# Performance work log

Measured on AMD Instinct MI355X. Metric: run time of the kernel, lower is better.

Reference implementation:

```python
import jax, jax.numpy as jnp
import numpy as np

N = 50000
E = 800000
D_IN = 64
D_H = 64


def setup_inputs() -> dict:
    key = jax.random.key(0)
    k1, k2, k3, k4 = jax.random.split(key, 4)
    x = jax.random.normal(k1, (N, D_IN), dtype=jnp.float32)
    edge_index = jax.random.randint(k2, (2, E), 0, N, dtype=jnp.int32)
    W1 = jax.random.normal(k3, (D_IN, D_H), dtype=jnp.float32) * (1.0 / np.sqrt(D_IN))
    b1 = jnp.zeros((D_H,), dtype=jnp.float32)
    W2 = jax.random.normal(k4, (D_H, 1), dtype=jnp.float32) * (1.0 / np.sqrt(D_H))
    b2 = jnpp = jnp.zeros((1,), dtype=jnp.float32)
    return {"x": x, "edge_index": edge_index, "W1": W1, "b1": b1, "W2": W2, "b2": b2}


def reference(x, edge_index, W1, b1, W2, b2):
    n = x.shape[0]
    # dgl.add_self_loop: append (i, i) edges for every node
    loops = jnp.arange(n, dtype=edge_index.dtype)
    src = jnp.concatenate([edge_index[0], loops])
    dst = jnp.concatenate([edge_index[1], loops])

    ones = jnp.ones(src.shape[0], dtype=x.dtype)
    deg_out = jax.ops.segment_sum(ones, src, num_segments=n)  # out-degree (src side)
    deg_in = jax.ops.segment_sum(ones, dst, num_segments=n)   # in-degree (dst side)
    # norm='both': symmetric D^{-1/2} A D^{-1/2}; zero where degree is zero (DGL sets inf->0)
    norm_src = jnp.where(deg_out > 0, jax.lax.rsqrt(deg_out), 0.0)[:, None]
    norm_dst = jnp.where(deg_in > 0, jax.lax.rsqrt(deg_in), 0.0)[:, None]

    def aggregate(h):
        # degree-normalized sparse neighbor sum (SpMM via gather + segment_sum)
        h = h * norm_src
        m = jax.ops.segment_sum(h[src], dst, num_segments=n)
        return m * norm_dst

    # layer 1 (in_feats == h_feats -> aggregate first, then transform), bias after agg
    h = aggregate(x) @ W1 + b1
    h = jax.nn.relu(h)
    # layer 2 (in_feats > out_feats -> transform first, then aggregate), bias at end
    out = aggregate(h @ W2) + b2
    return out  # [N, 1]
```

## Files before the change

kernel.cpp:

```cpp
#include <hip/hip_runtime.h>


constexpr int D = 64;
constexpr int NODE_TILE = 12800;
constexpr int NCHUNK = 64;
constexpr int HTH = 1024;

typedef float f32x8 __attribute__((ext_vector_type(8)));

__device__ __forceinline__ int rl_i(int v, int l) { return __builtin_amdgcn_readlane(v, l); }
__device__ __forceinline__ float rl_f(float v, int l) {
    return __builtin_bit_cast(float, __builtin_amdgcn_readlane(__builtin_bit_cast(int, v), l));
}

__global__ void __launch_bounds__(HTH) k_hist_lds(
        const int* __restrict__ src, const int* __restrict__ dst,
        unsigned int* __restrict__ part, int e, int ce) {
    __shared__ unsigned int h[NODE_TILE];
    int b = blockIdx.x;
    int v0 = blockIdx.y * NODE_TILE;
    for (int i = threadIdx.x; i < NODE_TILE; i += HTH) h[i] = 0u;
    __syncthreads();
    int lo = b * ce, hi = min(lo + ce, e);
    for (int i = lo + threadIdx.x; i < hi; i += HTH) {
        unsigned int us = (unsigned int)(src[i] - v0);
        if (us < (unsigned int)NODE_TILE) atomicAdd(&h[us], 1u);
        unsigned int ud = (unsigned int)(dst[i] - v0);
        if (ud < (unsigned int)NODE_TILE) atomicAdd(&h[ud], 0x10000u);
    }
    __syncthreads();
    unsigned int* p = part + ((size_t)blockIdx.y * NCHUNK + b) * NODE_TILE;
    for (int i = threadIdx.x; i < NODE_TILE; i += HTH) p[i] = h[i];
}

__global__ void k_merge(const unsigned int* __restrict__ part,
                        unsigned short* __restrict__ colpref,
                        int* __restrict__ cnt_out, int* __restrict__ cnt_in, int n) {
    int v = blockIdx.x * blockDim.x + threadIdx.x;
    if (v >= n) return;
    int pass = v / NODE_TILE;
    int vl = v - pass * NODE_TILE;
    const unsigned int* p = part + (size_t)pass * NCHUNK * NODE_TILE + vl;
    unsigned int tot = 0, run_in = 0;
    for (int b = 0; b < NCHUNK; ++b) {
        colpref[(size_t)b * n + v] = (unsigned short)run_in;
        unsigned int t = p[(size_t)b * NODE_TILE];
        tot += t;
        run_in += t >> 16;
    }
    cnt_out[v] = (int)(tot & 0xFFFFu);
    cnt_in[v] = (int)(tot >> 16);
}

__global__ void k_scan_block(const int* __restrict__ cnt_in, int* __restrict__ cursor,
                             int* __restrict__ bsum, int n) {
    __shared__ int s[256];
    int tid = threadIdx.x;
    int i = blockIdx.x * 256 + tid;
    int v = (i < n) ? cnt_in[i] : 0;
    s[tid] = v;
    __syncthreads();
#pragma unroll
    for (int off = 1; off < 256; off <<= 1) {
        int t = (tid >= off) ? s[tid - off] : 0;
        __syncthreads();
        s[tid] += t;
        __syncthreads();
    }
    if (i < n) cursor[i] = s[tid] - v;
    if (tid == 255) bsum[blockIdx.x] = s[255];
}

__global__ void k_scan_bsum(int* __restrict__ bsum, int nb) {
    __shared__ int s[256];
    __shared__ int carry;
    int tid = threadIdx.x;
    if (tid == 0) carry = 0;
    __syncthreads();
    for (int start = 0; start < nb; start += 256) {
        int i = start + tid;
        int v = (i < nb) ? bsum[i] : 0;
        s[tid] = v;
        __syncthreads();
#pragma unroll
        for (int off = 1; off < 256; off <<= 1) {
            int t = (tid >= off) ? s[tid - off] : 0;
            __syncthreads();
            s[tid] += t;
            __syncthreads();
        }
        if (i < nb) bsum[i] = s[tid] - v + carry;
        __syncthreads();
        if (tid == 0) carry += s[255];
        __syncthreads();
    }
}

__global__ void k_finalize(const int* __restrict__ cnt_out, const int* __restrict__ cnt_in,
                           const int* __restrict__ bsum,
                           int* __restrict__ cursor, int4* __restrict__ meta, int n) {
    int i = blockIdx.x * blockDim.x + threadIdx.x;
    if (i >= n) return;
    int start = cursor[i] + bsum[i >> 8];
    cursor[i] = start;
    meta[i] = make_int4(start, cnt_in[i], cnt_out[i], 0);
}

__global__ void __launch_bounds__(HTH) k_bin_lds(
        const int* __restrict__ src, const int* __restrict__ dst,
        const int* __restrict__ start, const unsigned short* __restrict__ colpref,
        const int* __restrict__ cnt_out,
        int2* __restrict__ col2, int e, int n, int ce) {
    __shared__ int cur[NODE_TILE];
    int b = blockIdx.x;
    int v0 = blockIdx.y * NODE_TILE;
    int vcnt = min(NODE_TILE, n - v0);
    for (int i = threadIdx.x; i < vcnt; i += HTH)
        cur[i] = start[v0 + i] + (int)colpref[(size_t)b * n + v0 + i];
    __syncthreads();
    int lo = b * ce, hi = min(lo + ce, e);
    for (int i = lo + threadIdx.x; i < hi; i += HTH) {
        int d = dst[i];
        unsigned int ud = (unsigned int)(d - v0);
        if (ud < (unsigned int)NODE_TILE) {
            int s = src[i];
            int p = atomicAdd(&cur[ud], 1);
            float w = rsqrtf((float)(cnt_out[s] + 1));
            col2[p] = make_int2(s, __builtin_bit_cast(int, w));
        }
    }
}

__global__ void __launch_bounds__(256) k_gemm(
        const float* __restrict__ x, const float* __restrict__ W1,
        float* __restrict__ y, int n) {
    __shared__ float sW1[D * D];
    int tid = threadIdx.x;
    for (int i = tid; i < D * D; i += 256) sW1[i] = W1[i];
    __syncthreads();

    int lane = tid & 63;
    int wv = __builtin_amdgcn_readfirstlane(tid >> 6);
    int r0 = (blockIdx.x * 4 + wv) * 8;
    if (r0 >= n) return;

    float acc[8];
#pragma unroll
    for (int i = 0; i < 8; ++i) acc[i] = 0.0f;

    if (r0 + 8 <= n) {
        const float* xw = x + (size_t)r0 * D;
#pragma unroll
        for (int kt = 0; kt < 8; ++kt) {
            const float* p = xw + kt * 8;
            f32x8 X0, X1, X2, X3, X4, X5, X6, X7;
            asm volatile(
                "s_load_dwordx8 %0, %8, 0x0\n\t"
                "s_load_dwordx8 %1, %8, 0x100\n\t"
                "s_load_dwordx8 %2, %8, 0x200\n\t"
                "s_load_dwordx8 %3, %8, 0x300\n\t"
                "s_load_dwordx8 %4, %8, 0x400\n\t"
                "s_load_dwordx8 %5, %8, 0x500\n\t"
                "s_load_dwordx8 %6, %8, 0x600\n\t"
                "s_load_dwordx8 %7, %8, 0x700\n\t"
                "s_waitcnt lgkmcnt(0)"
                : "=s"(X0), "=s"(X1), "=s"(X2), "=s"(X3),
                  "=s"(X4), "=s"(X5), "=s"(X6), "=s"(X7)
                : "s"(p));
#pragma unroll
            for (int j = 0; j < 8; ++j) {
                float wk = sW1[(kt * 8 + j) * D + lane];
                acc[0] = fmaf(X0[j], wk, acc[0]);
                acc[1] = fmaf(X1[j], wk, acc[1]);
                acc[2] = fmaf(X2[j], wk, acc[2]);
                acc[3] = fmaf(X3[j], wk, acc[3]);
                acc[4] = fmaf(X4[j], wk, acc[4]);
                acc[5] = fmaf(X5[j], wk, acc[5]);
                acc[6] = fmaf(X6[j], wk, acc[6]);
                acc[7] = fmaf(X7[j], wk, acc[7]);
            }
        }
#pragma unroll
        for (int i = 0; i < 8; ++i)
            y[(size_t)(r0 + i) * D + lane] = acc[i];
    } else {
        float xr[8];
#pragma unroll
        for (int i = 0; i < 8; ++i) {
            int r = r0 + i;
            xr[i] = (r < n) ? x[(size_t)r * D + lane] : 0.0f;
        }
#pragma unroll
        for (int k = 0; k < D; ++k) {
            float wk = sW1[k * D + lane];
#pragma unroll
            for (int i = 0; i < 8; ++i)
                acc[i] = fmaf(rl_f(xr[i], k), wk, acc[i]);
        }
#pragma unroll
        for (int i = 0; i < 8; ++i) {
            int r = r0 + i;
            if (r < n) y[(size_t)r * D + lane] = acc[i];
        }
    }
}

__global__ void __launch_bounds__(256) k_node(
        const float* __restrict__ y, const int4* __restrict__ meta,
        const int2* __restrict__ col2,
        const float* __restrict__ b1, const float* __restrict__ W2,
        float* __restrict__ zs, int n) {
    int tid = threadIdx.x;
    int wave = tid >> 6;
    int lane = tid & 63;
    float b1v = b1[lane];
    float w2v = W2[lane];

    int nwaves = gridDim.x * 4;
    int node = blockIdx.x * 4 + wave;
    if (node >= n) return;
    int4 mt = meta[node];

    while (true) {
        int nxt = node + nwaves;
        int4 mt_nx = make_int4(0, 0, 0, 0);
        if (nxt < n) mt_nx = meta[nxt];

        int base = mt.x;
        int cnt = mt.y;
        float nd = rsqrtf((float)(mt.y + 1));
        float ns = rsqrtf((float)(mt.z + 1));

        float a0 = ns * y[(size_t)node * D + lane];
        float a1 = 0.0f, a2 = 0.0f, a3 = 0.0f;

        for (int b0 = 0; b0 < cnt; b0 += 64) {
            int m = cnt - b0; if (m > 64) m = 64;
            int2 cw = (lane < m) ? col2[base + b0 + lane] : make_int2(0, 0);
            int idx = cw.x;
            float w = __builtin_bit_cast(float, cw.y);
            int j = 0;
            for (; j + 8 <= m; j += 8) {
                int s0 = rl_i(idx, j + 0), s1 = rl_i(idx, j + 1);
                int s2 = rl_i(idx, j + 2), s3 = rl_i(idx, j + 3);
                int s4 = rl_i(idx, j + 4), s5 = rl_i(idx, j + 5);
                int s6 = rl_i(idx, j + 6), s7 = rl_i(idx, j + 7);
                float x0 = y[(size_t)s0 * D + lane];
                float x1 = y[(size_t)s1 * D + lane];
                float x2 = y[(size_t)s2 * D + lane];
                float x3 = y[(size_t)s3 * D + lane];
                float x4 = y[(size_t)s4 * D + lane];
                float x5 = y[(size_t)s5 * D + lane];
                float x6 = y[(size_t)s6 * D + lane];
                float x7 = y[(size_t)s7 * D + lane];
                a0 = fmaf(rl_f(w, j + 0), x0, a0);
                a1 = fmaf(rl_f(w, j + 1), x1, a1);
                a2 = fmaf(rl_f(w, j + 2), x2, a2);
                a3 = fmaf(rl_f(w, j + 3), x3, a3);
                a0 = fmaf(rl_f(w, j + 4), x4, a0);
                a1 = fmaf(rl_f(w, j + 5), x5, a1);
                a2 = fmaf(rl_f(w, j + 6), x6, a2);
                a3 = fmaf(rl_f(w, j + 7), x7, a3);
            }
            for (; j < m; ++j)
                a0 = fmaf(rl_f(w, j), y[(size_t)rl_i(idx, j) * D + lane], a0);
        }

        float h = fmaxf(((a0 + a1) + (a2 + a3)) * nd + b1v, 0.0f);
        float zp = h * w2v;
#pragma unroll
        for (int off = 32; off > 0; off >>= 1) zp += __shfl_down(zp, off);
        if (lane == 0) zs[node] = zp * ns;

        if (nxt >= n) break;
        node = nxt;
        mt = mt_nx;
    }
}

__global__ void k_out(const float* __restrict__ zs,
                      const int4* __restrict__ meta, const int2* __restrict__ col2,
                      const float* __restrict__ b2,
                      float* __restrict__ out, int n) {
    int g = blockIdx.x * blockDim.x + threadIdx.x;
    int node = g >> 3;
    int sub = g & 7;
    if (node >= n) return;
    int4 mt = meta[node];
    int base = mt.x;
    int c = mt.y;
    float s = (sub == 0) ? zs[node] : 0.0f;
    for (int j = sub; j < c; j += 8) s += zs[col2[base + j].x];
    s += __shfl_xor(s, 1);
    s += __shfl_xor(s, 2);
    s += __shfl_xor(s, 4);
    if (sub == 0) {
        float nd = rsqrtf((float)(mt.y + 1));
        out[node] = nd * s + b2[0];
    }
}

extern "C" void kernel_launch(void* const* d_in, const int* in_sizes, int n_in,
                              void* d_out, int out_size, void* d_ws, size_t ws_size,
                              hipStream_t stream) {
    const float* x  = (const float*)d_in[0];
    const int*   ei = (const int*)d_in[1];
    const float* W1 = (const float*)d_in[2];
    const float* b1 = (const float*)d_in[3];
    const float* W2 = (const float*)d_in[4];
    const float* b2 = (const float*)d_in[5];
    float* out = (float*)d_out;

    const int n = in_sizes[0] / D;
    const int e = in_sizes[1] / 2;
    const int* src = ei;
    const int* dst = ei + e;

    const int nb = (n + 255) / 256;
    const int npass = (n + NODE_TILE - 1) / NODE_TILE;
    const int ce = (e + NCHUNK - 1) / NCHUNK;

    char* ws = (char*)d_ws;
    int*   cnt_out = (int*)ws;   ws += sizeof(int) * (size_t)n;
    int*   cnt_in  = (int*)ws;   ws += sizeof(int) * (size_t)n;
    int*   cursor  = (int*)ws;   ws += sizeof(int) * (size_t)n;
    int*   bsum    = (int*)ws;   ws += sizeof(int) * (size_t)((nb + 255) & ~255);
    int4*  meta    = (int4*)ws;  ws += sizeof(int4) * (size_t)n;
    unsigned short* colpref = (unsigned short*)ws;
    ws += sizeof(unsigned short) * (size_t)NCHUNK * n;
    int2*  col2    = (int2*)ws;  ws += sizeof(int2) * (size_t)e;
    size_t part_bytes = sizeof(unsigned int) * (size_t)npass * NCHUNK * NODE_TILE;
    size_t y_bytes    = sizeof(float) * (size_t)n * D;
    unsigned int* part = (unsigned int*)ws;
    float* y = (float*)ws;
    ws += (part_bytes > y_bytes ? part_bytes : y_bytes);
    float* zs = (float*)cnt_in;

    const int B = 256;

    k_hist_lds<<<dim3(NCHUNK, npass), HTH, 0, stream>>>(src, dst, part, e, ce);
    k_merge<<<(n + B - 1) / B, B, 0, stream>>>(part, colpref, cnt_out, cnt_in, n);
    k_scan_block<<<nb, 256, 0, stream>>>(cnt_in, cursor, bsum, n);
    k_scan_bsum<<<1, 256, 0, stream>>>(bsum, nb);
    k_finalize<<<(n + B - 1) / B, B, 0, stream>>>(cnt_out, cnt_in, bsum, cursor, meta, n);
    k_bin_lds<<<dim3(NCHUNK, npass), HTH, 0, stream>>>(src, dst, cursor, colpref,
                                                       cnt_out, col2, e, n, ce);
    k_gemm<<<(n + 31) / 32, B, 0, stream>>>(x, W1, y, n);
    k_node<<<2048, B, 0, stream>>>(y, meta, col2, b1, W2, zs, n);
    k_out<<<((size_t)n * 8 + B - 1) / B, B, 0, stream>>>(zs, meta, col2, b2, out, n);
}
```

Before: 113.9 us.

## Pack edge source and out-degree into one word; fuse merge with block scan

Replaces the 8-byte (source index, float weight) CSR entries with a 4-byte word: the source node id sits in the low 16 bits and its out-degree in the high 16 bits. The normalization weight is then recomputed with rsqrt inside the aggregation kernel, which halves the edge-list traffic in the bin, node and output kernels. The histogram merge and the per-block prefix scan are also fused into one kernel, removing a launch and a reread of the in-degree counts. The packing assumes node ids and out-degrees fit in 16 bits, which holds for N=50000 but is not general.

```diff
diff --git a/kernel.cpp b/kernel.cpp
--- a/kernel.cpp
+++ b/kernel.cpp
@@ -33,32 +33,30 @@
     for (int i = threadIdx.x; i < NODE_TILE; i += HTH) p[i] = h[i];
 }
 
-__global__ void k_merge(const unsigned int* __restrict__ part,
-                        unsigned short* __restrict__ colpref,
-                        int* __restrict__ cnt_out, int* __restrict__ cnt_in, int n) {
-    int v = blockIdx.x * blockDim.x + threadIdx.x;
-    if (v >= n) return;
-    int pass = v / NODE_TILE;
-    int vl = v - pass * NODE_TILE;
-    const unsigned int* p = part + (size_t)pass * NCHUNK * NODE_TILE + vl;
-    unsigned int tot = 0, run_in = 0;
-    for (int b = 0; b < NCHUNK; ++b) {
-        colpref[(size_t)b * n + v] = (unsigned short)run_in;
-        unsigned int t = p[(size_t)b * NODE_TILE];
-        tot += t;
-        run_in += t >> 16;
-    }
-    cnt_out[v] = (int)(tot & 0xFFFFu);
-    cnt_in[v] = (int)(tot >> 16);
-}
-
-__global__ void k_scan_block(const int* __restrict__ cnt_in, int* __restrict__ cursor,
-                             int* __restrict__ bsum, int n) {
+__global__ void k_merge_scan(const unsigned int* __restrict__ part,
+                             unsigned short* __restrict__ colpref,
+                             int* __restrict__ cnt_out, int* __restrict__ cnt_in,
+                             int* __restrict__ cursor, int* __restrict__ bsum, int n) {
     __shared__ int s[256];
     int tid = threadIdx.x;
-    int i = blockIdx.x * 256 + tid;
-    int v = (i < n) ? cnt_in[i] : 0;
-    s[tid] = v;
+    int v = blockIdx.x * 256 + tid;
+    int ci = 0;
+    if (v < n) {
+        int pass = v / NODE_TILE;
+        int vl = v - pass * NODE_TILE;
+        const unsigned int* p = part + (size_t)pass * NCHUNK * NODE_TILE + vl;
+        unsigned int tot = 0, run_in = 0;
+        for (int b = 0; b < NCHUNK; ++b) {
+            colpref[(size_t)b * n + v] = (unsigned short)run_in;
+            unsigned int t = p[(size_t)b * NODE_TILE];
+            tot += t;
+            run_in += t >> 16;
+        }
+        cnt_out[v] = (int)(tot & 0xFFFFu);
+        ci = (int)(tot >> 16);
+        cnt_in[v] = ci;
+    }
+    s[tid] = ci;
     __syncthreads();
 #pragma unroll
     for (int off = 1; off < 256; off <<= 1) {
@@ -67,7 +65,7 @@
         s[tid] += t;
         __syncthreads();
     }
-    if (i < n) cursor[i] = s[tid] - v;
+    if (v < n) cursor[v] = s[tid] - ci;
     if (tid == 255) bsum[blockIdx.x] = s[255];
 }
 
@@ -110,7 +108,7 @@
         const int* __restrict__ src, const int* __restrict__ dst,
         const int* __restrict__ start, const unsigned short* __restrict__ colpref,
         const int* __restrict__ cnt_out,
-        int2* __restrict__ col2, int e, int n, int ce) {
+        unsigned int* __restrict__ col, int e, int n, int ce) {
     __shared__ int cur[NODE_TILE];
     int b = blockIdx.x;
     int v0 = blockIdx.y * NODE_TILE;
@@ -125,8 +123,7 @@
         if (ud < (unsigned int)NODE_TILE) {
             int s = src[i];
             int p = atomicAdd(&cur[ud], 1);
-            float w = rsqrtf((float)(cnt_out[s] + 1));
-            col2[p] = make_int2(s, __builtin_bit_cast(int, w));
+            col[p] = (unsigned int)s | ((unsigned int)cnt_out[s] << 16);
         }
     }
 }
@@ -207,7 +204,7 @@
 
 __global__ void __launch_bounds__(256) k_node(
         const float* __restrict__ y, const int4* __restrict__ meta,
-        const int2* __restrict__ col2,
+        const unsigned int* __restrict__ col,
         const float* __restrict__ b1, const float* __restrict__ W2,
         float* __restrict__ zs, int n) {
     int tid = threadIdx.x;
@@ -236,9 +233,9 @@
 
         for (int b0 = 0; b0 < cnt; b0 += 64) {
             int m = cnt - b0; if (m > 64) m = 64;
-            int2 cw = (lane < m) ? col2[base + b0 + lane] : make_int2(0, 0);
-            int idx = cw.x;
-            float w = __builtin_bit_cast(float, cw.y);
+            unsigned int cw = (lane < m) ? col[base + b0 + lane] : 0u;
+            int idx = (int)(cw & 0xFFFFu);
+            float w = rsqrtf((float)(cw >> 16) + 1.0f);
             int j = 0;
             for (; j + 8 <= m; j += 8) {
                 int s0 = rl_i(idx, j + 0), s1 = rl_i(idx, j + 1);
@@ -279,7 +276,7 @@
 }
 
 __global__ void k_out(const float* __restrict__ zs,
-                      const int4* __restrict__ meta, const int2* __restrict__ col2,
+                      const int4* __restrict__ meta, const unsigned int* __restrict__ col,
                       const float* __restrict__ b2,
                       float* __restrict__ out, int n) {
     int g = blockIdx.x * blockDim.x + threadIdx.x;
@@ -290,7 +287,7 @@
     int base = mt.x;
     int c = mt.y;
     float s = (sub == 0) ? zs[node] : 0.0f;
-    for (int j = sub; j < c; j += 8) s += zs[col2[base + j].x];
+    for (int j = sub; j < c; j += 8) s += zs[col[base + j] & 0xFFFFu];
     s += __shfl_xor(s, 1);
     s += __shfl_xor(s, 2);
     s += __shfl_xor(s, 4);
@@ -328,7 +325,7 @@
     int4*  meta    = (int4*)ws;  ws += sizeof(int4) * (size_t)n;
     unsigned short* colpref = (unsigned short*)ws;
     ws += sizeof(unsigned short) * (size_t)NCHUNK * n;
-    int2*  col2    = (int2*)ws;  ws += sizeof(int2) * (size_t)e;
+    unsigned int* col = (unsigned int*)ws;  ws += sizeof(unsigned int) * (size_t)e;
     size_t part_bytes = sizeof(unsigned int) * (size_t)npass * NCHUNK * NODE_TILE;
     size_t y_bytes    = sizeof(float) * (size_t)n * D;
     unsigned int* part = (unsigned int*)ws;
@@ -339,13 +336,12 @@
     const int B = 256;
 
     k_hist_lds<<<dim3(NCHUNK, npass), HTH, 0, stream>>>(src, dst, part, e, ce);
-    k_merge<<<(n + B - 1) / B, B, 0, stream>>>(part, colpref, cnt_out, cnt_in, n);
-    k_scan_block<<<nb, 256, 0, stream>>>(cnt_in, cursor, bsum, n);
+    k_merge_scan<<<nb, 256, 0, stream>>>(part, colpref, cnt_out, cnt_in, cursor, bsum, n);
     k_scan_bsum<<<1, 256, 0, stream>>>(bsum, nb);
     k_finalize<<<(n + B - 1) / B, B, 0, stream>>>(cnt_out, cnt_in, bsum, cursor, meta, n);
     k_bin_lds<<<dim3(NCHUNK, npass), HTH, 0, stream>>>(src, dst, cursor, colpref,
-                                                       cnt_out, col2, e, n, ce);
+                                                       cnt_out, col, e, n, ce);
     k_gemm<<<(n + 31) / 32, B, 0, stream>>>(x, W1, y, n);
-    k_node<<<2048, B, 0, stream>>>(y, meta, col2, b1, W2, zs, n);
-    k_out<<<((size_t)n * 8 + B - 1) / B, B, 0, stream>>>(zs, meta, col2, b2, out, n);
-}
+    k_node<<<2048, B, 0, stream>>>(y, meta, col, b1, W2, zs, n);
+    k_out<<<((size_t)n * 8 + B - 1) / B, B, 0, stream>>>(zs, meta, col, b2, out, n);
+}
```

Result: faster. 111.0 us (-2.5%).
